# Kernel tuning notes

Measured on AMD Instinct MI355X. Metric: run time of the kernel, lower is better.

The kernel has to match this reference:

```python
import jax, jax.numpy as jnp
import numpy as np

V = 50000  # word vocab (table has V+1 rows)
L = 256    # number of labels
B = 128    # batch
T = 512    # sequence length


def setup_inputs() -> dict:
    key = jax.random.key(0)
    k1, k2, k3 = jax.random.split(key, 3)
    emis = jax.random.normal(k1, (V + 1, L), dtype=jnp.float32)
    trans = jax.random.normal(k2, (L, L), dtype=jnp.float32)
    words = jax.random.randint(k3, (B, T), 0, V, dtype=jnp.int32)
    return {"emis": emis, "trans": trans, "words": words}


def reference(emis, trans, words):
    # Gather all emission scores up front: [B, T, L]
    e = emis[words]
    alpha0 = e[:, 0]  # [B, L]

    def step(alpha_prev, e_t):
        # alpha_new[b, c] = logsumexp_p( e_t[b, c] + trans[c, p] + alpha_prev[b, p] )
        scores = e_t[:, :, None] + trans[None, :, :] + alpha_prev[:, None, :]  # [B, L, L]
        return jax.nn.logsumexp(scores, axis=2), None

    # scan over time: e[:, 1:] -> time-major [T-1, B, L]
    alpha_last, _ = jax.lax.scan(step, alpha0, jnp.swapaxes(e[:, 1:], 0, 1))
    log_Z = jax.nn.logsumexp(alpha_last, axis=1).sum()  # scalar, summed over batch
    return log_Z
```

## Files before the change

kernel.cpp:

```cpp
#include <hip/hip_runtime.h>

#define NB 128
#define NT 512
#define NL 256
#define NWG NB

typedef float f32x4 __attribute__((ext_vector_type(4)));
typedef int   i32x8 __attribute__((ext_vector_type(8)));

#define EASTRIDE 272
#define GEXP 7
#define E8M0_ONE 127
#define INV_LN2 1.4426950408889634f
#define LN2 0.6931471805599453f

__device__ inline float log2_fast(float x) {
#if __has_builtin(__builtin_amdgcn_logf)
    return __builtin_amdgcn_logf(x);
#else
    return __log2f(x);
#endif
}
__device__ inline float exp2_fast(float x) {
#if __has_builtin(__builtin_amdgcn_exp2f)
    return __builtin_amdgcn_exp2f(x);
#else
    return exp2f(x);
#endif
}

__device__ inline void barrier_lds_only() {
    asm volatile("s_waitcnt lgkmcnt(0)" ::: "memory");
    __builtin_amdgcn_s_barrier();
    asm volatile("" ::: "memory");
}

__device__ inline unsigned pk_fp8x4(float a, float b, float c, float d) {
    int w = __builtin_amdgcn_cvt_pk_fp8_f32(a, b, 0, false);
    w     = __builtin_amdgcn_cvt_pk_fp8_f32(c, d, w, true);
    return (unsigned)w;
}

__global__ __launch_bounds__(512, 2) void crf_forward(
    const float* __restrict__ emis,
    const float* __restrict__ trans,
    const int*   __restrict__ words,
    float*       __restrict__ bout)
{
    const int tid = threadIdx.x;
    const int l   = tid & 63;
    const int wv  = tid >> 6;
    const int g   = l >> 4;
    const int b   = l & 15;

    __shared__ __align__(16) unsigned char ea[2][EASTRIDE];
    __shared__ __align__(16) float pm[2][8];

    const int* ws = words + (size_t)blockIdx.x * NT;
    const int eoff = wv * 32 + g * 4;

    i32x8 afr[2][2];
    #pragma unroll
    for (int T = 0; T < 2; ++T) {
        const int row = wv * 32 + T * 16 + b;
        #pragma unroll
        for (int kt = 0; kt < 2; ++kt) {
            const float* src = trans + row * NL + kt * 128 + g * 32;
            i32x8 a;
            #pragma unroll
            for (int w = 0; w < 8; ++w) {
                float4 v = *reinterpret_cast<const float4*>(src + w * 4);
                a[w] = (int)pk_fp8x4(__expf(v.x), __expf(v.y),
                                     __expf(v.z), __expf(v.w));
            }
            afr[T][kt] = a;
        }
    }

    const int w0 = ws[0];
    const int w1 = ws[1];
    const int w2 = ws[2];
    int wA = ws[3];
    int wB = ws[4];

    float S = 0.f;

    {
        const float* e0 = emis + (size_t)w0 * NL + eoff;
        f32x4 v0 = *reinterpret_cast<const f32x4*>(e0);
        f32x4 v1 = *reinterpret_cast<const f32x4*>(e0 + 16);
        float p00 = exp2_fast(v0[0] * INV_LN2), p01 = exp2_fast(v0[1] * INV_LN2);
        float p02 = exp2_fast(v0[2] * INV_LN2), p03 = exp2_fast(v0[3] * INV_LN2);
        float p10 = exp2_fast(v1[0] * INV_LN2), p11 = exp2_fast(v1[1] * INV_LN2);
        float p12 = exp2_fast(v1[2] * INV_LN2), p13 = exp2_fast(v1[3] * INV_LN2);
        float pmax = fmaxf(fmaxf(fmaxf(p00, p01), fmaxf(p02, p03)),
                           fmaxf(fmaxf(p10, p11), fmaxf(p12, p13)));
        pmax = fmaxf(pmax, __shfl_xor(pmax, 16));
        pmax = fmaxf(pmax, __shfl_xor(pmax, 32));
        if (l == 0) pm[0][wv] = pmax;
        if (b == 0) {
            *reinterpret_cast<unsigned*>(&ea[0][wv * 32 + g * 4]) =
                pk_fp8x4(p00, p01, p02, p03);
            *reinterpret_cast<unsigned*>(&ea[0][wv * 32 + 16 + g * 4]) =
                pk_fp8x4(p10, p11, p12, p13);
        }
    }
    f32x4 pfA0, pfA1, pfB0, pfB1;
    {
        const float* p1 = emis + (size_t)w1 * NL + eoff;
        pfA0 = *reinterpret_cast<const f32x4*>(p1);
        pfA1 = *reinterpret_cast<const f32x4*>(p1 + 16);
        const float* p2 = emis + (size_t)w2 * NL + eoff;
        pfB0 = *reinterpret_cast<const f32x4*>(p2);
        pfB1 = *reinterpret_cast<const f32x4*>(p2 + 16);
    }
    barrier_lds_only();

#define CRF_STEP(t, RD, WR, PF0, PF1, WREG)                                     \
    {                                                                           \
                         \
        i32x8 bq0 = *reinterpret_cast<const i32x8*>(&ea[RD][g * 32]);           \
        i32x8 bq1 = *reinterpret_cast<const i32x8*>(&ea[RD][128 + g * 32]);     \
        f32x4 pm0 = *reinterpret_cast<const f32x4*>(&pm[RD][0]);                \
        f32x4 pm1 = *reinterpret_cast<const f32x4*>(&pm[RD][4]);                \
        float gm = fmaxf(fmaxf(fmaxf(pm0[0], pm0[1]), fmaxf(pm0[2], pm0[3])),   \
                         fmaxf(fmaxf(pm1[0], pm1[1]), fmaxf(pm1[2], pm1[3])));  \
        int   kb = (int)(__builtin_bit_cast(unsigned, gm) >> 23) - (127 - GEXP);\
        S += (float)kb;                                                         \
        float kbf = (float)kb;                                                  \
             \
        float exa0 = exp2_fast(fmaf(PF0[0], INV_LN2, -kbf));                    \
        float exa1 = exp2_fast(fmaf(PF0[1], INV_LN2, -kbf));                    \
        float exa2 = exp2_fast(fmaf(PF0[2], INV_LN2, -kbf));                    \
        float exa3 = exp2_fast(fmaf(PF0[3], INV_LN2, -kbf));                    \
        float exb0 = exp2_fast(fmaf(PF1[0], INV_LN2, -kbf));                    \
        float exb1 = exp2_fast(fmaf(PF1[1], INV_LN2, -kbf));                    \
        float exb2 = exp2_fast(fmaf(PF1[2], INV_LN2, -kbf));                    \
        float exb3 = exp2_fast(fmaf(PF1[3], INV_LN2, -kbf));                    \
        if ((t) + 2 < NT) {                                                     \
            const float* ep = emis + (size_t)WREG * NL + eoff;                  \
            PF0 = *reinterpret_cast<const f32x4*>(ep);                          \
            PF1 = *reinterpret_cast<const f32x4*>(ep + 16);                     \
        }                                                                       \
        if ((t) + 4 < NT) WREG = ws[(t) + 4];                                   \
                         \
        f32x4 z0 = {0.f, 0.f, 0.f, 0.f};                                        \
        f32x4 z1 = {0.f, 0.f, 0.f, 0.f};                                        \
        z0 = __builtin_amdgcn_mfma_scale_f32_16x16x128_f8f6f4(                  \
                 afr[0][0], bq0, z0, 0, 0, 0, E8M0_ONE, 0, E8M0_ONE);           \
        z1 = __builtin_amdgcn_mfma_scale_f32_16x16x128_f8f6f4(                  \
                 afr[1][0], bq0, z1, 0, 0, 0, E8M0_ONE, 0, E8M0_ONE);           \
        z0 = __builtin_amdgcn_mfma_scale_f32_16x16x128_f8f6f4(                  \
                 afr[0][1], bq1, z0, 0, 0, 0, E8M0_ONE, 0, E8M0_ONE);           \
        z1 = __builtin_amdgcn_mfma_scale_f32_16x16x128_f8f6f4(                  \
                 afr[1][1], bq1, z1, 0, 0, 0, E8M0_ONE, 0, E8M0_ONE);           \
        float v00 = z0[0] * exa0, v01 = z0[1] * exa1;                           \
        float v02 = z0[2] * exa2, v03 = z0[3] * exa3;                           \
        float v10 = z1[0] * exb0, v11 = z1[1] * exb1;                           \
        float v12 = z1[2] * exb2, v13 = z1[3] * exb3;                           \
        float pmax = fmaxf(fmaxf(fmaxf(v00, v01), fmaxf(v02, v03)),             \
                           fmaxf(fmaxf(v10, v11), fmaxf(v12, v13)));            \
        pmax = fmaxf(pmax, __shfl_xor(pmax, 16));                               \
        pmax = fmaxf(pmax, __shfl_xor(pmax, 32));                               \
        if (l == 0) pm[WR][wv] = pmax;                                          \
        if (b == 0) {                                                           \
            *reinterpret_cast<unsigned*>(&ea[WR][wv * 32 + g * 4]) =            \
                pk_fp8x4(v00, v01, v02, v03);                                   \
            *reinterpret_cast<unsigned*>(&ea[WR][wv * 32 + 16 + g * 4]) =       \
                pk_fp8x4(v10, v11, v12, v13);                                   \
        }                                                                       \
        barrier_lds_only();                                                     \
    }

    for (int t = 1; t + 1 < NT; t += 2) {
        CRF_STEP(t,     0, 1, pfA0, pfA1, wA);
        CRF_STEP(t + 1, 1, 0, pfB0, pfB1, wB);
    }
    CRF_STEP(511, 0, 1, pfA0, pfA1, wA);
#undef CRF_STEP

    if (tid < 64) {
        unsigned u = *reinterpret_cast<const unsigned*>(&ea[1][tid * 4]);
        float s = __builtin_amdgcn_cvt_f32_fp8((int)u, 0)
                + __builtin_amdgcn_cvt_f32_fp8((int)u, 1)
                + __builtin_amdgcn_cvt_f32_fp8((int)u, 2)
                + __builtin_amdgcn_cvt_f32_fp8((int)u, 3);
        #pragma unroll
        for (int off = 32; off; off >>= 1) s += __shfl_xor(s, off);
        if (tid == 0) bout[blockIdx.x] = (S + log2_fast(s)) * LN2;
    }
}

__global__ void crf_reduce(const float* __restrict__ bout, float* __restrict__ out)
{
    const int tid = threadIdx.x;
    float v = bout[tid];
    #pragma unroll
    for (int off = 32; off; off >>= 1) v += __shfl_xor(v, off);
    __shared__ float sred[2];
    if ((tid & 63) == 0) sred[tid >> 6] = v;
    __syncthreads();
    if (tid == 0) out[0] = sred[0] + sred[1];
}

extern "C" void kernel_launch(void* const* d_in, const int* in_sizes, int n_in,
                              void* d_out, int out_size, void* d_ws, size_t ws_size,
                              hipStream_t stream)
{
    const float* emis  = (const float*)d_in[0];
    const float* trans = (const float*)d_in[1];
    const int*   words = (const int*)d_in[2];
    float* out  = (float*)d_out;
    float* bout = (float*)d_ws;

    crf_forward<<<NWG, 512, 0, stream>>>(emis, trans, words, bout);
    crf_reduce<<<1, NB, 0, stream>>>(bout, out);
}
```

Baseline: 308.2 us.

## Defer per-step max reduction off critical path using lagged scale exponent

Moves the cross-lane max reduction of each step's results out of the serial step: the max is computed after the barrier in the next step, and the scale exponent is derived from the max two steps back, with a clamp at 440 to keep FP8 values in range. It also permutes the K ordering of the transition fragments so each lane writes its two FP8 words as one 64-bit LDS store and reads B operands from a fixed offset. It also hoists the word-index load earlier. This shortens the per-step dependency chain between MFMA output and barrier, at the cost of a stale normalisation that relies on clamping to avoid overflow and may lose precision.

```diff
diff --git a/kernel.cpp b/kernel.cpp
--- a/kernel.cpp
+++ b/kernel.cpp
@@ -59,19 +59,20 @@
     const int* ws = words + (size_t)blockIdx.x * NT;
     const int eoff = wv * 32 + g * 4;
 
+    static const int coff[8] = {0, 16, 4, 20, 8, 24, 12, 28};
     i32x8 afr[2][2];
     #pragma unroll
     for (int T = 0; T < 2; ++T) {
         const int row = wv * 32 + T * 16 + b;
         #pragma unroll
         for (int kt = 0; kt < 2; ++kt) {
-            const float* src = trans + row * NL + kt * 128 + g * 32;
+            const float* src = trans + row * NL + (kt * 4 + g) * 32;
             i32x8 a;
             #pragma unroll
-            for (int w = 0; w < 8; ++w) {
-                float4 v = *reinterpret_cast<const float4*>(src + w * 4);
-                a[w] = (int)pk_fp8x4(__expf(v.x), __expf(v.y),
-                                     __expf(v.z), __expf(v.w));
+            for (int jj = 0; jj < 8; ++jj) {
+                float4 v = *reinterpret_cast<const float4*>(src + coff[jj]);
+                a[jj] = (int)pk_fp8x4(__expf(v.x), __expf(v.y),
+                                      __expf(v.z), __expf(v.w));
             }
             afr[T][kt] = a;
         }
@@ -84,6 +85,8 @@
     int wB = ws[4];
 
     float S = 0.f;
+    int   kbp = GEXP;
+    float mprev;
 
     {
         const float* e0 = emis + (size_t)w0 * NL + eoff;
@@ -93,16 +96,16 @@
         float p02 = exp2_fast(v0[2] * INV_LN2), p03 = exp2_fast(v0[3] * INV_LN2);
         float p10 = exp2_fast(v1[0] * INV_LN2), p11 = exp2_fast(v1[1] * INV_LN2);
         float p12 = exp2_fast(v1[2] * INV_LN2), p13 = exp2_fast(v1[3] * INV_LN2);
-        float pmax = fmaxf(fmaxf(fmaxf(p00, p01), fmaxf(p02, p03)),
-                           fmaxf(fmaxf(p10, p11), fmaxf(p12, p13)));
-        pmax = fmaxf(pmax, __shfl_xor(pmax, 16));
-        pmax = fmaxf(pmax, __shfl_xor(pmax, 32));
-        if (l == 0) pm[0][wv] = pmax;
+        mprev = fmaxf(fmaxf(fmaxf(p00, p01), fmaxf(p02, p03)),
+                      fmaxf(fmaxf(p10, p11), fmaxf(p12, p13)));
+        float gmax = fmaxf(mprev, __shfl_xor(mprev, 16));
+        gmax = fmaxf(gmax, __shfl_xor(gmax, 32));
+        if (l == 0) { pm[0][wv] = gmax; pm[1][wv] = gmax; }
         if (b == 0) {
-            *reinterpret_cast<unsigned*>(&ea[0][wv * 32 + g * 4]) =
-                pk_fp8x4(p00, p01, p02, p03);
-            *reinterpret_cast<unsigned*>(&ea[0][wv * 32 + 16 + g * 4]) =
-                pk_fp8x4(p10, p11, p12, p13);
+            unsigned q0 = pk_fp8x4(p00, p01, p02, p03);
+            unsigned q1 = pk_fp8x4(p10, p11, p12, p13);
+            *reinterpret_cast<unsigned long long*>(&ea[0][wv * 32 + g * 8]) =
+                ((unsigned long long)q1 << 32) | q0;
         }
     }
     f32x4 pfA0, pfA1, pfB0, pfB1;
@@ -116,19 +119,28 @@
     }
     barrier_lds_only();
 
-#define CRF_STEP(t, RD, WR, PF0, PF1, WREG)                                     \
+#define CRF_STEP(t, EARD, EAWR, PMRD, PMWR, PF0, PF1, WREG)                     \
     {                                                                           \
-                         \
-        i32x8 bq0 = *reinterpret_cast<const i32x8*>(&ea[RD][g * 32]);           \
-        i32x8 bq1 = *reinterpret_cast<const i32x8*>(&ea[RD][128 + g * 32]);     \
-        f32x4 pm0 = *reinterpret_cast<const f32x4*>(&pm[RD][0]);                \
-        f32x4 pm1 = *reinterpret_cast<const f32x4*>(&pm[RD][4]);                \
+                    \
+        int wnext = 0;                                                          \
+        if ((t) + 4 < NT) wnext = ws[(t) + 4];                                  \
+                                           \
+        i32x8 bq0 = *reinterpret_cast<const i32x8*>(&ea[EARD][0]);              \
+        i32x8 bq1 = *reinterpret_cast<const i32x8*>(&ea[EARD][128]);            \
+        f32x4 pm0 = *reinterpret_cast<const f32x4*>(&pm[PMRD][0]);              \
+        f32x4 pm1 = *reinterpret_cast<const f32x4*>(&pm[PMRD][4]);              \
+          \
+        float m1 = fmaxf(mprev, __shfl_xor(mprev, 16));                         \
+        m1 = fmaxf(m1, __shfl_xor(m1, 32));                                     \
+        if (l == 0) pm[PMWR][wv] = m1;                                          \
         float gm = fmaxf(fmaxf(fmaxf(pm0[0], pm0[1]), fmaxf(pm0[2], pm0[3])),   \
                          fmaxf(fmaxf(pm1[0], pm1[1]), fmaxf(pm1[2], pm1[3])));  \
-        int   kb = (int)(__builtin_bit_cast(unsigned, gm) >> 23) - (127 - GEXP);\
+        int kb = ((int)(__builtin_bit_cast(unsigned, gm) >> 23) - 127)          \
+                 + 2 * GEXP - kbp;                                              \
+        kbp = kb;                                                               \
         S += (float)kb;                                                         \
         float kbf = (float)kb;                                                  \
-             \
+                                   \
         float exa0 = exp2_fast(fmaf(PF0[0], INV_LN2, -kbf));                    \
         float exa1 = exp2_fast(fmaf(PF0[1], INV_LN2, -kbf));                    \
         float exa2 = exp2_fast(fmaf(PF0[2], INV_LN2, -kbf));                    \
@@ -142,7 +154,7 @@
             PF0 = *reinterpret_cast<const f32x4*>(ep);                          \
             PF1 = *reinterpret_cast<const f32x4*>(ep + 16);                     \
         }                                                                       \
-        if ((t) + 4 < NT) WREG = ws[(t) + 4];                                   \
+        WREG = wnext;                                                           \
                          \
         f32x4 z0 = {0.f, 0.f, 0.f, 0.f};                                        \
         f32x4 z1 = {0.f, 0.f, 0.f, 0.f};                                        \
@@ -154,29 +166,28 @@
                  afr[0][1], bq1, z0, 0, 0, 0, E8M0_ONE, 0, E8M0_ONE);           \
         z1 = __builtin_amdgcn_mfma_scale_f32_16x16x128_f8f6f4(                  \
                  afr[1][1], bq1, z1, 0, 0, 0, E8M0_ONE, 0, E8M0_ONE);           \
-        float v00 = z0[0] * exa0, v01 = z0[1] * exa1;                           \
-        float v02 = z0[2] * exa2, v03 = z0[3] * exa3;                           \
-        float v10 = z1[0] * exb0, v11 = z1[1] * exb1;                           \
-        float v12 = z1[2] * exb2, v13 = z1[3] * exb3;                           \
-        float pmax = fmaxf(fmaxf(fmaxf(v00, v01), fmaxf(v02, v03)),             \
-                           fmaxf(fmaxf(v10, v11), fmaxf(v12, v13)));            \
-        pmax = fmaxf(pmax, __shfl_xor(pmax, 16));                               \
-        pmax = fmaxf(pmax, __shfl_xor(pmax, 32));                               \
-        if (l == 0) pm[WR][wv] = pmax;                                          \
+        float v00 = fminf(z0[0] * exa0, 440.f), v01 = fminf(z0[1] * exa1, 440.f);\
+        float v02 = fminf(z0[2] * exa2, 440.f), v03 = fminf(z0[3] * exa3, 440.f);\
+        float v10 = fminf(z1[0] * exb0, 440.f), v11 = fminf(z1[1] * exb1, 440.f);\
+        float v12 = fminf(z1[2] * exb2, 440.f), v13 = fminf(z1[3] * exb3, 440.f);\
         if (b == 0) {                                                           \
-            *reinterpret_cast<unsigned*>(&ea[WR][wv * 32 + g * 4]) =            \
-                pk_fp8x4(v00, v01, v02, v03);                                   \
-            *reinterpret_cast<unsigned*>(&ea[WR][wv * 32 + 16 + g * 4]) =       \
-                pk_fp8x4(v10, v11, v12, v13);                                   \
+            unsigned q0 = pk_fp8x4(v00, v01, v02, v03);                         \
+            unsigned q1 = pk_fp8x4(v10, v11, v12, v13);                         \
+            *reinterpret_cast<unsigned long long*>(                             \
+                &ea[EAWR][wv * 32 + g * 8]) =                                   \
+                ((unsigned long long)q1 << 32) | q0;                            \
         }                                                                       \
+              \
+        mprev = fmaxf(fmaxf(fmaxf(v00, v01), fmaxf(v02, v03)),                  \
+                      fmaxf(fmaxf(v10, v11), fmaxf(v12, v13)));                 \
         barrier_lds_only();                                                     \
     }
 
     for (int t = 1; t + 1 < NT; t += 2) {
-        CRF_STEP(t,     0, 1, pfA0, pfA1, wA);
-        CRF_STEP(t + 1, 1, 0, pfB0, pfB1, wB);
-    }
-    CRF_STEP(511, 0, 1, pfA0, pfA1, wA);
+        CRF_STEP(t,     0, 1, 1, 0, pfA0, pfA1, wA);
+        CRF_STEP(t + 1, 1, 0, 0, 1, pfB0, pfB1, wB);
+    }
+    CRF_STEP(511, 0, 1, 1, 0, pfA0, pfA1, wA);
 #undef CRF_STEP
 
     if (tid < 64) {
```

Result: slower. 323.3 us (+4.9%).
